# Performance work log

Measured on AMD Instinct MI355X. Metric: run time of the kernel, lower is better.

Reference implementation:

```python
import jax, jax.numpy as jnp
import numpy as np

EPS = 1e-7
FEAT_DIM = 128
N_DATA = 100000
NCE_K = 16384
NCE_T = 0.07


def _l2norm(x):
    # Normalize(power=2): x / (sum(x^2, axis=1)^(1/2))
    return x / jnp.sqrt(jnp.sum(x * x, axis=1, keepdims=True))


def _embed(x, W, b):
    return _l2norm(x @ W.T + b)


def _contrast_loss(x, n_data):
    # x: [B, K+1] of (unnormalized) probabilities; col 0 = positive
    bsz = x.shape[0]
    m = x.shape[1] - 1
    Pn = 1.0 / float(n_data)
    c = m * Pn + EPS
    log_D1 = jnp.log(x[:, 0] / (x[:, 0] + c))          # positives
    log_D0 = jnp.log((m * Pn) / (x[:, 1:] + c))         # negatives
    return -(log_D1.sum() + log_D0.sum()) / bsz


def setup_inputs() -> dict:
    key = jax.random.key(0)
    ks = jax.random.split(key, 10)
    s_dim, t_dim = 1024, 2048
    B = 64
    stdv = 1.0 / np.sqrt(FEAT_DIM / 3.0)
    inp = {
        "f_s": jax.random.normal(ks[0], (B, s_dim), dtype=jnp.float32),
        "f_t": jax.random.normal(ks[1], (B, t_dim), dtype=jnp.float32),
        "idx": jax.random.randint(ks[2], (B,), 0, N_DATA),
        "contrast_idx": jax.random.randint(ks[3], (B, NCE_K + 1), 0, N_DATA),
        # Embed params (linear): Linear(dim_in, feat_dim)
        "Ws": jax.random.normal(ks[4], (FEAT_DIM, s_dim), dtype=jnp.float32) / np.sqrt(s_dim),
        "bs": jnp.zeros((FEAT_DIM,), dtype=jnp.float32),
        "Wt": jax.random.normal(ks[5], (FEAT_DIM, t_dim), dtype=jnp.float32) / np.sqrt(t_dim),
        "bt": jnp.zeros((FEAT_DIM,), dtype=jnp.float32),
        # memory banks, init uniform(-stdv, stdv) as in CRD ContrastMemory
        "memory_v1": jax.random.uniform(ks[6], (N_DATA, FEAT_DIM), jnp.float32, -stdv, stdv),
        "memory_v2": jax.random.uniform(ks[7], (N_DATA, FEAT_DIM), jnp.float32, -stdv, stdv),
    }
    return inp


def reference(f_s, f_t, idx, contrast_idx, Ws, bs, Wt, bt, memory_v1, memory_v2):
    v_s = _embed(f_s, Ws, bs)   # [B, D]
    v_t = _embed(f_t, Wt, bt)   # [B, D]

    # idx.select(1,0).copy_(y): column 0 is the positive index
    idx_all = jnp.concatenate([idx[:, None], contrast_idx[:, 1:]], axis=1)  # [B, K+1]

    # gather from memory banks + bmm similarity
    w1 = memory_v1[idx_all]   # [B, K+1, D] (v_t side bank)
    w2 = memory_v2[idx_all]   # [B, K+1, D] (v_s side bank)
    out_t = jnp.exp(jnp.einsum('bkd,bd->bk', w1, v_t) / NCE_T)  # out_v2
    out_s = jnp.exp(jnp.einsum('bkd,bd->bk', w2, v_s) / NCE_T)  # out_v1

    # Z set on first batch: Z = out.mean() * n_data (detached constant)
    Z_s = jax.lax.stop_gradient(out_s.mean()) * N_DATA
    Z_t = jax.lax.stop_gradient(out_t.mean()) * N_DATA
    out_s = out_s / Z_s
    out_t = out_t / Z_t

    s_loss = _contrast_loss(out_s, N_DATA)
    t_loss = _contrast_loss(out_t, N_DATA)
    return s_loss + t_loss
```

## Files before the change

kernel.cpp:

```cpp
#include <hip/hip_runtime.h>

#define NDATA 100000
#define KP1 16385
#define BSZ 64
#define PTOT (BSZ * KP1)
#define NCHUNKS 6250
#define INV_T (1.0f / 0.07f)
#define OVF_CAP 256
#define NMBLK 1024
#define ACC_STRIDE 64
#define ACC_GROUPS 32

typedef short short8 __attribute__((ext_vector_type(8)));
typedef float f32x4 __attribute__((ext_vector_type(4)));

__device__ __forceinline__ float wave_reduce64(float v) {
    #pragma unroll
    for (int off = 32; off >= 1; off >>= 1) v += __shfl_xor(v, off);
    return v;
}

__device__ __forceinline__ float group_reduce16(float v) {
    v += __shfl_xor(v, 8); v += __shfl_xor(v, 4);
    v += __shfl_xor(v, 2); v += __shfl_xor(v, 1);
    return v;
}

__device__ __forceinline__ unsigned short f2bf(float f) {
    unsigned u = __float_as_uint(f);
    u += 0x7FFFu + ((u >> 16) & 1u);
    return (unsigned short)(u >> 16);
}

__device__ __forceinline__ float bfm(float x) {
    return __uint_as_float(((unsigned)f2bf(x)) << 16);
}

__device__ __forceinline__ short8 pack_bf16(float4 lo, float4 hi) {
    short8 r;
    r[0] = (short)f2bf(lo.x); r[1] = (short)f2bf(lo.y);
    r[2] = (short)f2bf(lo.z); r[3] = (short)f2bf(lo.w);
    r[4] = (short)f2bf(hi.x); r[5] = (short)f2bf(hi.y);
    r[6] = (short)f2bf(hi.z); r[7] = (short)f2bf(hi.w);
    return r;
}

__device__ __forceinline__ float dot4(float4 a, float4 b, float acc) {
    acc = fmaf(a.x, b.x, acc);
    acc = fmaf(a.y, b.y, acc);
    acc = fmaf(a.z, b.z, acc);
    return fmaf(a.w, b.w, acc);
}

__device__ __forceinline__ float dot8bf(const float4* a, const float4* v, int li, float d) {
    #pragma unroll
    for (int h = 0; h < 2; ++h) {
        const float4 x = a[li * 2 + h], y = v[li * 2 + h];
        d = fmaf(bfm(x.x), bfm(y.x), d);
        d = fmaf(bfm(x.y), bfm(y.y), d);
        d = fmaf(bfm(x.z), bfm(y.z), d);
        d = fmaf(bfm(x.w), bfm(y.w), d);
    }
    return d;
}

__global__ __launch_bounds__(256) void embed_kernel(
    const float* __restrict__ fs, const float* __restrict__ ft,
    const float* __restrict__ Ws, const float* __restrict__ bs,
    const float* __restrict__ Wt, const float* __restrict__ bt,
    float* __restrict__ vraw_s, float* __restrict__ vraw_t)
{
    __shared__ __align__(16) float4 FS[512];
    __shared__ __align__(16) float4 FT[1024];

    const int t  = threadIdx.x;
    const int b0 = blockIdx.y * 2;

    for (int q = t; q < 512; q += 256) {
        const int b = q >> 8, i = q & 255;
        FS[q] = ((const float4*)(fs + (size_t)(b0 + b) * 1024))[i];
    }
    for (int q = t; q < 1024; q += 256) {
        const int b = q >> 9, i = q & 511;
        FT[q] = ((const float4*)(ft + (size_t)(b0 + b) * 2048))[i];
    }
    __syncthreads();

    const int w = t >> 6, lane = t & 63;
    const int d = blockIdx.x * 4 + w;

    {
        const float4* wrow = (const float4*)(Ws + (size_t)d * 1024);
        float a0 = 0.0f, a1 = 0.0f;
        #pragma unroll
        for (int i = 0; i < 4; ++i) {
            const float4 wv = wrow[i * 64 + lane];
            a0 = dot4(wv, FS[i * 64 + lane], a0);
            a1 = dot4(wv, FS[256 + i * 64 + lane], a1);
        }
        a0 = wave_reduce64(a0) + bs[d];
        a1 = wave_reduce64(a1) + bs[d];
        if (lane == 0) {
            vraw_s[(size_t)b0 * 128 + d]       = a0;
            vraw_s[(size_t)(b0 + 1) * 128 + d] = a1;
        }
    }
    {
        const float4* wrow = (const float4*)(Wt + (size_t)d * 2048);
        float a0 = 0.0f, a1 = 0.0f;
        #pragma unroll
        for (int i = 0; i < 8; ++i) {
            const float4 wv = wrow[i * 64 + lane];
            a0 = dot4(wv, FT[i * 64 + lane], a0);
            a1 = dot4(wv, FT[512 + i * 64 + lane], a1);
        }
        a0 = wave_reduce64(a0) + bt[d];
        a1 = wave_reduce64(a1) + bt[d];
        if (lane == 0) {
            vraw_t[(size_t)b0 * 128 + d]       = a0;
            vraw_t[(size_t)(b0 + 1) * 128 + d] = a1;
        }
    }
}

__global__ __launch_bounds__(256) void norm_kernel(
    const float* __restrict__ vraw_t, const float* __restrict__ vraw_s,
    float* __restrict__ sct, float* __restrict__ scs)
{
    const float* __restrict__ v = blockIdx.x ? vraw_s : vraw_t;
    float* __restrict__ sc      = blockIdx.x ? scs : sct;
    const int t = threadIdx.x, b = t >> 2, g = t & 3;
    const float4* row = (const float4*)(v + (size_t)b * 128 + g * 32);
    float s = 0.0f;
    #pragma unroll
    for (int j = 0; j < 8; ++j) s = dot4(row[j], row[j], s);
    s += __shfl_xor(s, 1);
    s += __shfl_xor(s, 2);
    if (g == 0) sc[b] = INV_T * rsqrtf(s);
}

__global__ __launch_bounds__(256) void mask_kernel(
    const int* __restrict__ cidx,
    unsigned long long* __restrict__ rowmask,
    unsigned* __restrict__ ovfcnt, unsigned* __restrict__ ovf)
{
    const int b = blockIdx.x, part = blockIdx.y, t = threadIdx.x;
    __shared__ unsigned lcnt;
    __shared__ unsigned lbuf[OVF_CAP];
    if (t == 0) lcnt = 0;
    __syncthreads();

    const unsigned long long bit = 1ull << b;
    const int kbase = part * 1024 + 1;
    #pragma unroll
    for (int j = 0; j < 4; ++j) {
        const int row = cidx[(size_t)b * KP1 + kbase + j * 256 + t];
        const unsigned long long old = atomicOr(&rowmask[row], bit);
        if (old & bit) {
            const unsigned p = atomicAdd(&lcnt, 1u);
            if (p < OVF_CAP) lbuf[p] = ((unsigned)b << 17) | (unsigned)row;
        }
    }
    __syncthreads();
    const int blk = b * 16 + part;
    const unsigned n = min(lcnt, (unsigned)OVF_CAP);
    if (t == 0) ovfcnt[blk] = n;
    for (unsigned q = t; q < n; q += 256) ovf[(size_t)blk * OVF_CAP + q] = lbuf[q];
}

__global__ __launch_bounds__(256) void sgemm_kernel(
    const float* __restrict__ m1, const float* __restrict__ m2,
    const float* __restrict__ vraw_s, const float* __restrict__ vraw_t,
    const float* __restrict__ sct, const float* __restrict__ scs,
    const unsigned long long* __restrict__ rowmask,
    float* __restrict__ acc)
{
    const int t = threadIdx.x;
    const int bank = blockIdx.y;
    const float* __restrict__ bankp = bank ? m2 : m1;
    const float* __restrict__ vp    = bank ? vraw_s : vraw_t;
    const float* __restrict__ scp   = bank ? scs : sct;

    const int lane = t & 63;
    const int m  = lane & 15;
    const int q4 = lane >> 4;

    short8 bfv[4][4];
    #pragma unroll
    for (int n = 0; n < 4; ++n) {
        const float4* vrow = (const float4*)(vp + (size_t)(n * 16 + m) * 128);
        #pragma unroll
        for (int kk = 0; kk < 4; ++kk) {
            const float4 lo = vrow[(kk * 4 + q4) * 2];
            const float4 hi = vrow[(kk * 4 + q4) * 2 + 1];
            bfv[n][kk] = pack_bf16(lo, hi);
        }
    }

    f32x4 scv[4];
    #pragma unroll
    for (int n = 0; n < 4; ++n) scv[n] = ((const f32x4*)scp)[n * 4 + q4];

    float se = 0.0f, se2 = 0.0f;

    const int wave   = (blockIdx.x << 2) | (t >> 6);
    const int nwaves = gridDim.x << 2;

    for (int cid = wave; cid < NCHUNKS; cid += nwaves) {
        const int row0 = cid << 4;
        const float4* arow = (const float4*)(bankp + (size_t)(row0 + m) * 128);

        float4 a[8];
        #pragma unroll
        for (int kk = 0; kk < 4; ++kk) {
            a[kk * 2]     = arow[(kk * 4 + q4) * 2];
            a[kk * 2 + 1] = arow[(kk * 4 + q4) * 2 + 1];
        }
        short8 af[4];
        #pragma unroll
        for (int kk = 0; kk < 4; ++kk)
            af[kk] = pack_bf16(a[kk * 2], a[kk * 2 + 1]);

        const unsigned long long msk = rowmask[row0 + m];

        #pragma unroll
        for (int n = 0; n < 4; ++n) {
            f32x4 av = {0.f, 0.f, 0.f, 0.f};
            #pragma unroll
            for (int kk = 0; kk < 4; ++kk)
                av = __builtin_amdgcn_mfma_f32_16x16x32_bf16(bfv[n][kk], af[kk], av, 0, 0, 0);
            const int base_b = n * 16 + q4 * 4;
            #pragma unroll
            for (int j = 0; j < 4; ++j) {
                const float mj = (float)((unsigned)((msk >> (base_b + j)) & 1ull));
                const float e = __expf(av[j] * scv[n][j]) * mj;
                se += e;
                se2 = fmaf(e, e, se2);
            }
        }
    }

    se  = wave_reduce64(se);
    se2 = wave_reduce64(se2);
    __shared__ float red[4][2];
    if (lane == 0) { red[t >> 6][0] = se; red[t >> 6][1] = se2; }
    __syncthreads();
    if (t < 2) {
        const float s = red[0][t] + red[1][t] + red[2][t] + red[3][t];
        atomicAdd(&acc[(blockIdx.x & (ACC_GROUPS - 1)) * ACC_STRIDE + bank * 2 + t], s);
    }
}

__global__ __launch_bounds__(256) void ovf_kernel(
    const unsigned* __restrict__ ovfcnt, const unsigned* __restrict__ ovf,
    const float* __restrict__ m1, const float* __restrict__ m2,
    const float* __restrict__ vraw_t, const float* __restrict__ vraw_s,
    const float* __restrict__ sct, const float* __restrict__ scs,
    float* __restrict__ acc)
{
    const int blk = blockIdx.x, t = threadIdx.x;
    const int cnt = (int)ovfcnt[blk];
    const int wave = t >> 6, lane = t & 63, g = lane >> 4, li = lane & 15;

    float seT = 0.f, se2T = 0.f, seS = 0.f, se2S = 0.f;

    for (int i0 = 0; i0 * 16 < cnt; ++i0) {
        const int e = i0 * 16 + wave * 4 + g;
        const bool ok = e < cnt;
        const unsigned ue = ovf[(size_t)blk * OVF_CAP + (ok ? e : 0)];
        const int b = (int)(ue >> 17), row = (int)(ue & 0x1FFFFu);

        float dT = dot8bf((const float4*)(m1 + (size_t)row * 128),
                          (const float4*)(vraw_t + (size_t)b * 128), li, 0.f);
        float dS = dot8bf((const float4*)(m2 + (size_t)row * 128),
                          (const float4*)(vraw_s + (size_t)b * 128), li, 0.f);
        dT = group_reduce16(dT);
        dS = group_reduce16(dS);
        if (ok && li == 0) {
            const float eT = __expf(dT * sct[b]);
            const float eS = __expf(dS * scs[b]);
            seT += eT; se2T = fmaf(eT, eT, se2T);
            seS += eS; se2S = fmaf(eS, eS, se2S);
        }
    }

    seT = wave_reduce64(seT);  se2T = wave_reduce64(se2T);
    seS = wave_reduce64(seS);  se2S = wave_reduce64(se2S);
    __shared__ float red[4][4];
    if (lane == 0) {
        red[wave][0] = seT; red[wave][1] = se2T; red[wave][2] = seS; red[wave][3] = se2S;
    }
    __syncthreads();
    if (t < 4)
        atomicAdd(&acc[(blk & (ACC_GROUPS - 1)) * ACC_STRIDE + t],
                  red[0][t] + red[1][t] + red[2][t] + red[3][t]);
}

__global__ __launch_bounds__(256) void final_kernel(
    const int* __restrict__ idx,
    const float* __restrict__ m1, const float* __restrict__ m2,
    const float* __restrict__ vraw_t, const float* __restrict__ vraw_s,
    const float* __restrict__ sct, const float* __restrict__ scs,
    const float* __restrict__ acc, float* __restrict__ out)
{
    const int t = threadIdx.x, wave = t >> 6, lane = t & 63, g = lane >> 4, li = lane & 15;
    __shared__ float e1s[64], e2s[64];

    #pragma unroll
    for (int i = 0; i < 4; ++i) {
        const int b = wave * 16 + i * 4 + g;
        const int row = idx[b];
        float dT = dot8bf((const float4*)(m1 + (size_t)row * 128),
                          (const float4*)(vraw_t + (size_t)b * 128), li, 0.f);
        float dS = dot8bf((const float4*)(m2 + (size_t)row * 128),
                          (const float4*)(vraw_s + (size_t)b * 128), li, 0.f);
        dT = group_reduce16(dT);
        dS = group_reduce16(dS);
        if (li == 0) {
            e1s[b] = __expf(dT * sct[b]);
            e2s[b] = __expf(dS * scs[b]);
        }
    }
    __syncthreads();

    if (t < 64) {
        const int b = t;
        const float c = 0.16384f + 1e-7f;
        const float e1p = e1s[b], e2p = e2s[b];

        const float pseT = wave_reduce64(e1p);
        const float pseS = wave_reduce64(e2p);

        float seT_neg = 0.f, se2T_neg = 0.f, seS_neg = 0.f, se2S_neg = 0.f;
        for (int s = 0; s < ACC_GROUPS; ++s) {
            seT_neg  += acc[s * ACC_STRIDE + 0];
            se2T_neg += acc[s * ACC_STRIDE + 1];
            seS_neg  += acc[s * ACC_STRIDE + 2];
            se2S_neg += acc[s * ACC_STRIDE + 3];
        }

        const float zn = (float)PTOT / (float)NDATA;
        const float invZt = zn / (seT_neg + pseT);
        const float invZs = zn / (seS_neg + pseS);

        const float PB = (float)(PTOT - BSZ);
        const float LOG_MPN_C = -6.1035156e-7f;
        const float ic = 1.0f / c;

        const float negT = PB * LOG_MPN_C
                         - seT_neg * invZt * ic
                         + 0.5f * se2T_neg * invZt * invZt * ic * ic;
        const float negS = PB * LOG_MPN_C
                         - seS_neg * invZs * ic
                         + 0.5f * se2S_neg * invZs * invZs * ic * ic;

        const float x0t = e1p * invZt, x0s = e2p * invZs;
        float pos = __logf(x0t / (x0t + c)) + __logf(x0s / (x0s + c));
        pos = wave_reduce64(pos);

        if (b == 0) out[0] = -(negT + negS + pos) * (1.0f / 64.0f);
    }
}

extern "C" void kernel_launch(void* const* d_in, const int* in_sizes, int n_in,
                              void* d_out, int out_size, void* d_ws, size_t ws_size,
                              hipStream_t stream) {
    const float* fs   = (const float*)d_in[0];
    const float* ft   = (const float*)d_in[1];
    const int*   idx  = (const int*)d_in[2];
    const int*   cidx = (const int*)d_in[3];
    const float* Ws   = (const float*)d_in[4];
    const float* bs   = (const float*)d_in[5];
    const float* Wt   = (const float*)d_in[6];
    const float* bt   = (const float*)d_in[7];
    const float* m1   = (const float*)d_in[8];
    const float* m2   = (const float*)d_in[9];
    float* out = (float*)d_out;

    float* ws     = (float*)d_ws;
    float* sct    = ws;
    float* scs    = ws + 64;
    float* acc    = ws + 128;
    unsigned long long* rowmask = (unsigned long long*)(ws + 4096);
    unsigned* ovfcnt = (unsigned*)(ws + 204096);
    unsigned* ovf    = (unsigned*)(ws + 205120);
    float* vraw_s = ws + 467264;
    float* vraw_t = ws + 475456;

    hipMemsetAsync(ws + 128, 0, (size_t)(205120 - 128) * sizeof(float), stream);

    embed_kernel<<<dim3(32, 32), dim3(256), 0, stream>>>(
        fs, ft, Ws, bs, Wt, bt, vraw_s, vraw_t);
    norm_kernel<<<dim3(2), dim3(256), 0, stream>>>(
        vraw_t, vraw_s, sct, scs);
    mask_kernel<<<dim3(64, 16), dim3(256), 0, stream>>>(
        cidx, rowmask, ovfcnt, ovf);
    sgemm_kernel<<<dim3(521, 2), dim3(256), 0, stream>>>(
        m1, m2, vraw_s, vraw_t, sct, scs, rowmask, acc);
    ovf_kernel<<<dim3(NMBLK), dim3(256), 0, stream>>>(
        ovfcnt, ovf, m1, m2, vraw_t, vraw_s, sct, scs, acc);
    final_kernel<<<dim3(1), dim3(256), 0, stream>>>(
        idx, m1, m2, vraw_t, vraw_s, sct, scs, acc, out);
}
```

Before: 230.4 us.

## Replace bitmask plus overflow pass with per-row byte-count histogram and double-buffered sgemm

Swaps the per-row 64-bit occurrence mask and its separate overflow kernel for a histogram of 8-bit counts per (row, batch), packed four to a word. The sgemm weights each exp term by its count, so duplicates are handled in the main pass and the ovf kernel is removed. The sgemm loop now uses a fixed 256x2 grid with manual double-buffered prefetch of bank rows and counts. The cost is a much larger workspace memset (about 6.4MB instead of 0.8MB) and more count-load traffic, and 8-bit counters could overflow if one row repeats more than 255 times within a single batch.

```diff
diff --git a/kernel.cpp b/kernel.cpp
--- a/kernel.cpp
+++ b/kernel.cpp
@@ -6,10 +6,10 @@
 #define PTOT (BSZ * KP1)
 #define NCHUNKS 6250
 #define INV_T (1.0f / 0.07f)
-#define OVF_CAP 256
-#define NMBLK 1024
 #define ACC_STRIDE 64
 #define ACC_GROUPS 32
+#define SG_NWAVES 1024
+#define SG_NITER 7
 
 typedef short short8 __attribute__((ext_vector_type(8)));
 typedef float f32x4 __attribute__((ext_vector_type(4)));
@@ -139,40 +139,64 @@
     if (g == 0) sc[b] = INV_T * rsqrtf(s);
 }
 
-__global__ __launch_bounds__(256) void mask_kernel(
-    const int* __restrict__ cidx,
-    unsigned long long* __restrict__ rowmask,
-    unsigned* __restrict__ ovfcnt, unsigned* __restrict__ ovf)
+__global__ __launch_bounds__(256) void hist_kernel(
+    const int* __restrict__ cidx, unsigned* __restrict__ cnt)
 {
     const int b = blockIdx.x, part = blockIdx.y, t = threadIdx.x;
-    __shared__ unsigned lcnt;
-    __shared__ unsigned lbuf[OVF_CAP];
-    if (t == 0) lcnt = 0;
-    __syncthreads();
-
-    const unsigned long long bit = 1ull << b;
+    const unsigned inc = 1u << ((b & 3) * 8);
+    const int w = b >> 2;
     const int kbase = part * 1024 + 1;
     #pragma unroll
     for (int j = 0; j < 4; ++j) {
         const int row = cidx[(size_t)b * KP1 + kbase + j * 256 + t];
-        const unsigned long long old = atomicOr(&rowmask[row], bit);
-        if (old & bit) {
-            const unsigned p = atomicAdd(&lcnt, 1u);
-            if (p < OVF_CAP) lbuf[p] = ((unsigned)b << 17) | (unsigned)row;
-        }
-    }
-    __syncthreads();
-    const int blk = b * 16 + part;
-    const unsigned n = min(lcnt, (unsigned)OVF_CAP);
-    if (t == 0) ovfcnt[blk] = n;
-    for (unsigned q = t; q < n; q += 256) ovf[(size_t)blk * OVF_CAP + q] = lbuf[q];
-}
+        atomicAdd(&cnt[(size_t)row * 16 + w], inc);
+    }
+}
+
+#define SG_ISSUE(AB, CB, VM, CID)                                            \
+  {                                                                          \
+    const int cc_ = ((CID) < NCHUNKS) ? (CID) : (NCHUNKS - 1);               \
+    VM = ((CID) < NCHUNKS) ? ~0u : 0u;                                       \
+    const int r0_ = cc_ << 4;                                                \
+    const float4* ar_ = (const float4*)(bankp + (size_t)(r0_ + m) * 128);    \
+    _Pragma("unroll")                                                        \
+    for (int kk = 0; kk < 4; ++kk) {                                         \
+      AB[kk * 2]     = ar_[(kk * 4 + q4) * 2];                               \
+      AB[kk * 2 + 1] = ar_[(kk * 4 + q4) * 2 + 1];                           \
+    }                                                                        \
+    _Pragma("unroll")                                                        \
+    for (int n = 0; n < 4; ++n)                                              \
+      CB[n] = cnt[(size_t)(r0_ + m) * 16 + n * 4 + q4];                      \
+  }
+
+#define SG_PROCESS(AB, CB, VM)                                               \
+  {                                                                          \
+    short8 af_[4];                                                           \
+    _Pragma("unroll")                                                        \
+    for (int kk = 0; kk < 4; ++kk)                                           \
+      af_[kk] = pack_bf16(AB[kk * 2], AB[kk * 2 + 1]);                       \
+    _Pragma("unroll")                                                        \
+    for (int n = 0; n < 4; ++n) {                                            \
+      f32x4 av = {0.f, 0.f, 0.f, 0.f};                                       \
+      _Pragma("unroll")                                                      \
+      for (int kk = 0; kk < 4; ++kk)                                         \
+        av = __builtin_amdgcn_mfma_f32_16x16x32_bf16(bfv[n][kk], af_[kk], av, 0, 0, 0); \
+      const unsigned cw_ = CB[n] & VM;                                       \
+      _Pragma("unroll")                                                      \
+      for (int j = 0; j < 4; ++j) {                                          \
+        const float fm_ = (float)((cw_ >> (8 * j)) & 255u);                  \
+        const float e_  = __expf(av[j] * scv[n][j]);                         \
+        se  = fmaf(e_, fm_, se);                                             \
+        se2 = fmaf(e_ * fm_, e_, se2);                                       \
+      }                                                                      \
+    }                                                                        \
+  }
 
 __global__ __launch_bounds__(256) void sgemm_kernel(
     const float* __restrict__ m1, const float* __restrict__ m2,
     const float* __restrict__ vraw_s, const float* __restrict__ vraw_t,
     const float* __restrict__ sct, const float* __restrict__ scs,
-    const unsigned long long* __restrict__ rowmask,
+    const unsigned* __restrict__ cnt,
     float* __restrict__ acc)
 {
     const int t = threadIdx.x;
@@ -203,42 +227,20 @@
 
     float se = 0.0f, se2 = 0.0f;
 
-    const int wave   = (blockIdx.x << 2) | (t >> 6);
-    const int nwaves = gridDim.x << 2;
-
-    for (int cid = wave; cid < NCHUNKS; cid += nwaves) {
-        const int row0 = cid << 4;
-        const float4* arow = (const float4*)(bankp + (size_t)(row0 + m) * 128);
-
-        float4 a[8];
-        #pragma unroll
-        for (int kk = 0; kk < 4; ++kk) {
-            a[kk * 2]     = arow[(kk * 4 + q4) * 2];
-            a[kk * 2 + 1] = arow[(kk * 4 + q4) * 2 + 1];
-        }
-        short8 af[4];
-        #pragma unroll
-        for (int kk = 0; kk < 4; ++kk)
-            af[kk] = pack_bf16(a[kk * 2], a[kk * 2 + 1]);
-
-        const unsigned long long msk = rowmask[row0 + m];
-
-        #pragma unroll
-        for (int n = 0; n < 4; ++n) {
-            f32x4 av = {0.f, 0.f, 0.f, 0.f};
-            #pragma unroll
-            for (int kk = 0; kk < 4; ++kk)
-                av = __builtin_amdgcn_mfma_f32_16x16x32_bf16(bfv[n][kk], af[kk], av, 0, 0, 0);
-            const int base_b = n * 16 + q4 * 4;
-            #pragma unroll
-            for (int j = 0; j < 4; ++j) {
-                const float mj = (float)((unsigned)((msk >> (base_b + j)) & 1ull));
-                const float e = __expf(av[j] * scv[n][j]) * mj;
-                se += e;
-                se2 = fmaf(e, e, se2);
-            }
-        }
-    }
+    const int wave = (blockIdx.x << 2) | (t >> 6);
+
+    float4 aA[8], aB[8];
+    unsigned cA[4], cB[4], vmA, vmB;
+
+    SG_ISSUE(aA, cA, vmA, wave);
+    #pragma unroll
+    for (int p = 0; p < (SG_NITER - 1) / 2; ++p) {
+        SG_ISSUE(aB, cB, vmB, wave + (2 * p + 1) * SG_NWAVES);
+        SG_PROCESS(aA, cA, vmA);
+        SG_ISSUE(aA, cA, vmA, wave + (2 * p + 2) * SG_NWAVES);
+        SG_PROCESS(aB, cB, vmB);
+    }
+    SG_PROCESS(aA, cA, vmA);
 
     se  = wave_reduce64(se);
     se2 = wave_reduce64(se2);
@@ -249,51 +251,6 @@
         const float s = red[0][t] + red[1][t] + red[2][t] + red[3][t];
         atomicAdd(&acc[(blockIdx.x & (ACC_GROUPS - 1)) * ACC_STRIDE + bank * 2 + t], s);
     }
-}
-
-__global__ __launch_bounds__(256) void ovf_kernel(
-    const unsigned* __restrict__ ovfcnt, const unsigned* __restrict__ ovf,
-    const float* __restrict__ m1, const float* __restrict__ m2,
-    const float* __restrict__ vraw_t, const float* __restrict__ vraw_s,
-    const float* __restrict__ sct, const float* __restrict__ scs,
-    float* __restrict__ acc)
-{
-    const int blk = blockIdx.x, t = threadIdx.x;
-    const int cnt = (int)ovfcnt[blk];
-    const int wave = t >> 6, lane = t & 63, g = lane >> 4, li = lane & 15;
-
-    float seT = 0.f, se2T = 0.f, seS = 0.f, se2S = 0.f;
-
-    for (int i0 = 0; i0 * 16 < cnt; ++i0) {
-        const int e = i0 * 16 + wave * 4 + g;
-        const bool ok = e < cnt;
-        const unsigned ue = ovf[(size_t)blk * OVF_CAP + (ok ? e : 0)];
-        const int b = (int)(ue >> 17), row = (int)(ue & 0x1FFFFu);
-
-        float dT = dot8bf((const float4*)(m1 + (size_t)row * 128),
-                          (const float4*)(vraw_t + (size_t)b * 128), li, 0.f);
-        float dS = dot8bf((const float4*)(m2 + (size_t)row * 128),
-                          (const float4*)(vraw_s + (size_t)b * 128), li, 0.f);
-        dT = group_reduce16(dT);
-        dS = group_reduce16(dS);
-        if (ok && li == 0) {
-            const float eT = __expf(dT * sct[b]);
-            const float eS = __expf(dS * scs[b]);
-            seT += eT; se2T = fmaf(eT, eT, se2T);
-            seS += eS; se2S = fmaf(eS, eS, se2S);
-        }
-    }
-
-    seT = wave_reduce64(seT);  se2T = wave_reduce64(se2T);
-    seS = wave_reduce64(seS);  se2S = wave_reduce64(se2S);
-    __shared__ float red[4][4];
-    if (lane == 0) {
-        red[wave][0] = seT; red[wave][1] = se2T; red[wave][2] = seS; red[wave][3] = se2S;
-    }
-    __syncthreads();
-    if (t < 4)
-        atomicAdd(&acc[(blk & (ACC_GROUPS - 1)) * ACC_STRIDE + t],
-                  red[0][t] + red[1][t] + red[2][t] + red[3][t]);
 }
 
 __global__ __launch_bounds__(256) void final_kernel(
@@ -381,24 +338,20 @@
     float* sct    = ws;
     float* scs    = ws + 64;
     float* acc    = ws + 128;
-    unsigned long long* rowmask = (unsigned long long*)(ws + 4096);
-    unsigned* ovfcnt = (unsigned*)(ws + 204096);
-    unsigned* ovf    = (unsigned*)(ws + 205120);
-    float* vraw_s = ws + 467264;
-    float* vraw_t = ws + 475456;
-
-    hipMemsetAsync(ws + 128, 0, (size_t)(205120 - 128) * sizeof(float), stream);
+    unsigned* cnt = (unsigned*)(ws + 4096);
+    float* vraw_s = ws + 1604096;
+    float* vraw_t = ws + 1612288;
+
+    hipMemsetAsync(ws + 128, 0, (size_t)(1604096 - 128) * sizeof(float), stream);
 
     embed_kernel<<<dim3(32, 32), dim3(256), 0, stream>>>(
         fs, ft, Ws, bs, Wt, bt, vraw_s, vraw_t);
     norm_kernel<<<dim3(2), dim3(256), 0, stream>>>(
         vraw_t, vraw_s, sct, scs);
-    mask_kernel<<<dim3(64, 16), dim3(256), 0, stream>>>(
-        cidx, rowmask, ovfcnt, ovf);
-    sgemm_kernel<<<dim3(521, 2), dim3(256), 0, stream>>>(
-        m1, m2, vraw_s, vraw_t, sct, scs, rowmask, acc);
-    ovf_kernel<<<dim3(NMBLK), dim3(256), 0, stream>>>(
-        ovfcnt, ovf, m1, m2, vraw_t, vraw_s, sct, scs, acc);
+    hist_kernel<<<dim3(64, 16), dim3(256), 0, stream>>>(
+        cidx, cnt);
+    sgemm_kernel<<<dim3(256, 2), dim3(256), 0, stream>>>(
+        m1, m2, vraw_s, vraw_t, sct, scs, cnt, acc);
     final_kernel<<<dim3(1), dim3(256), 0, stream>>>(
         idx, m1, m2, vraw_t, vraw_s, sct, scs, acc, out);
 }
```

Measured after the change: 212.3 us. 7.8% less time.
